# Kernel tuning notes

Hardware: AMD Instinct MI355X
Metric: run time of the kernel (lower is better)

Reference implementation:

```python
import jax, jax.numpy as jnp
import numpy as np

BS, T, N_AGENTS, N_ACTIONS = 8, 256, 8, 20
A = N_AGENTS * N_ACTIONS          # 160 gru input dim
E, D, HID, S = 128, 128, 32, 256  # encoder_dim, decoder_dim, mixing_embed_dim, state_dim
EMBED = HID * (A + E)             # 9216


def _lin(k, out_d, in_d):
    s = 1.0 / np.sqrt(in_d)
    return jax.random.uniform(k, (out_d, in_d), jnp.float32, -s, s)


def _vec(k, d, fan):
    s = 1.0 / np.sqrt(fan)
    return jax.random.uniform(k, (d,), jnp.float32, -s, s)


def setup_inputs() -> dict:
    key = jax.random.key(0)
    ks = jax.random.split(key, 32)
    inp = {
        'act': jax.random.uniform(ks[0], (BS, T, N_AGENTS, N_ACTIONS), jnp.float32),
        'states': jax.random.normal(ks[1], (BS, T, S), jnp.float32),
        # GRU (PyTorch layout: gates stacked [r; z; n])
        'gru_wih': _lin(ks[2], 3 * E, A),
        'gru_whh': _lin(ks[3], 3 * E, E),
        'gru_bih': _vec(ks[4], 3 * E, E),
        'gru_bhh': _vec(ks[5], 3 * E, E),
        # encoder fc
        'fc_w': _lin(ks[6], D, E),
        'fc_b': _vec(ks[7], D, E),
        # attention
        'attn_w': _lin(ks[8], D, D + E),
        'v_w': _vec(ks[9], D, D),
        # hyper_w_1 (2-layer MLP)
        'hw1_w0': _lin(ks[10], EMBED, S), 'hw1_b0': _vec(ks[11], EMBED, S),
        'hw1_w1': _lin(ks[12], EMBED, EMBED), 'hw1_b1': _vec(ks[13], EMBED, EMBED),
        # hyper_w_final (2-layer MLP)
        'hwf_w0': _lin(ks[14], HID, S), 'hwf_b0': _vec(ks[15], HID, S),
        'hwf_w1': _lin(ks[16], HID, HID), 'hwf_b1': _vec(ks[17], HID, HID),
        # hyper_b_1
        'hb1_w': _lin(ks[18], HID, S), 'hb1_b': _vec(ks[19], HID, S),
        # hyper_b_2 (2-layer MLP)
        'hb2_w0': _lin(ks[20], HID, S), 'hb2_b0': _vec(ks[21], HID, S),
        'hb2_w1': _lin(ks[22], 1, HID), 'hb2_b1': _vec(ks[23], 1, HID),
    }
    return inp


def reference(act, states, gru_wih, gru_whh, gru_bih, gru_bhh, fc_w, fc_b,
              attn_w, v_w, hw1_w0, hw1_b0, hw1_w1, hw1_b1,
              hwf_w0, hwf_b0, hwf_w1, hwf_b1, hb1_w, hb1_b,
              hb2_w0, hb2_b0, hb2_w1, hb2_b1):
    bs, t, n_ag, n_ac = act.shape
    a = n_ag * n_ac
    e = gru_whh.shape[1]
    d = fc_w.shape[0]
    hid = hb1_w.shape[0]

    act_flat = act.reshape(bs, t, a)
    # act_his = [zeros, act]; prefixes use only the first t steps of it
    x = jnp.concatenate([jnp.zeros((bs, 1, a), act.dtype), act_flat[:, : t - 1]], axis=1)

    # GRU over full sequence once (causal => identical to recomputing each prefix)
    def step(h, xt):
        gi = xt @ gru_wih.T + gru_bih
        gh = h @ gru_whh.T + gru_bhh
        ir, iz, i_n = jnp.split(gi, 3, axis=-1)
        hr, hz, h_n = jnp.split(gh, 3, axis=-1)
        r = jax.nn.sigmoid(ir + hr)
        z = jax.nn.sigmoid(iz + hz)
        n = jnp.tanh(i_n + r * h_n)
        h_new = (1.0 - z) * n + z * h
        return h_new, h_new

    h0 = jnp.zeros((bs, e), act.dtype)
    _, enc = jax.lax.scan(step, h0, jnp.swapaxes(x, 0, 1))
    enc = jnp.swapaxes(enc, 0, 1)  # [bs, T, E]

    # s0 for prefix ending at step q is tanh(fc(enc[:, q]))
    s0 = jnp.tanh(enc @ fc_w.T + fc_b)  # [bs, T, D]

    # attention: cat order is (s, enc_output)
    w_s, w_e = attn_w[:, :d], attn_w[:, d:]
    ps = s0 @ w_s.T            # [bs, Tq, D]
    pe = enc @ w_e.T           # [bs, Tk, D]
    pre = jnp.tanh(ps[:, :, None, :] + pe[:, None, :, :])  # [bs, Tq, Tk, D]
    scores = jnp.einsum('bqkd,d->bqk', pre, v_w)
    mask = jnp.tril(jnp.ones((t, t), bool))  # key j <= query q (prefix j < idx)
    scores = jnp.where(mask[None], scores, -jnp.inf)
    attn = jax.nn.softmax(scores, axis=-1)
    c = jnp.einsum('bqk,bke->bqe', attn, enc)  # [bs, T, E]

    inp = jnp.concatenate([act_flat, c], axis=-1).reshape(bs * t, 1, a + e)
    st = states.reshape(bs * t, -1)

    w1 = (jax.nn.relu(st @ hw1_w0.T + hw1_b0) @ hw1_w1.T + hw1_b1).reshape(bs * t, a + e, hid)
    b1 = (st @ hb1_w.T + hb1_b)[:, None, :]
    h = jax.nn.relu(jnp.einsum('bik,bkh->bih', inp, w1) + b1)  # [bs*T, 1, hid]

    wf = (jax.nn.relu(st @ hwf_w0.T + hwf_b0) @ hwf_w1.T + hwf_b1)[:, :, None]  # [bs*T, hid, 1]
    b2 = (jax.nn.relu(st @ hb2_w0.T + hb2_b0) @ hb2_w1.T + hb2_b1)[:, :, None]  # [bs*T, 1, 1]
    q = (jnp.einsum('bih,bho->bio', h, wf) + b2).reshape(bs, t, 1)
    return q
```

## Files before the change

kernel.cpp:

```cpp
#include <hip/hip_runtime.h>
#include <hip/hip_bf16.h>
#include <stdint.h>

typedef __attribute__((ext_vector_type(4))) float f32x4;
typedef __attribute__((ext_vector_type(8))) short short8v;
typedef __attribute__((ext_vector_type(4))) unsigned short u16x4;

constexpr int kT  = 256;
constexpr int kA  = 160;

__device__ __forceinline__ float bf2f(unsigned short u){
  union { unsigned int u; float f; } c; c.u = ((unsigned int)u) << 16; return c.f;
}
__device__ __forceinline__ unsigned short f2bf(float f){
  union { float f; unsigned int u; } c; c.f = f;
  unsigned int r = (c.u + 0x7FFFu + ((c.u >> 16) & 1u)) >> 16;
  return (unsigned short)r;
}
__device__ __forceinline__ float sigmoid_fast(float x){
  return __builtin_amdgcn_rcpf(1.f + __expf(-x));
}
__device__ __forceinline__ float tanhf_fast(float x){
  float xc = fminf(fmaxf(x, -15.f), 15.f);
  float t = __expf(2.f * xc);
  return (t - 1.f) * __builtin_amdgcn_rcpf(t + 1.f);
}
__device__ __forceinline__ void gload_lds16(const void* g, void* l){
  __builtin_amdgcn_global_load_lds((const __attribute__((address_space(1))) void*)g,
                                   (__attribute__((address_space(3))) void*)l, 16, 0, 0);
}
__device__ __forceinline__ void bar_lgkm(){
  asm volatile("s_waitcnt lgkmcnt(0)" ::: "memory");
  __builtin_amdgcn_s_barrier();
  asm volatile("" ::: "memory");
}
__device__ __forceinline__ void bar_only(){
  asm volatile("" ::: "memory");
  __builtin_amdgcn_s_barrier();
  asm volatile("" ::: "memory");
}

__global__ __launch_bounds__(256) void k_fill_f32(float* out, int n, float v){
  int i = blockIdx.x * blockDim.x + threadIdx.x;
  if (i < n) out[i] = v;
}

__global__ __launch_bounds__(256) void k_f32_to_bf16(const float* __restrict__ src,
                                                     unsigned short* __restrict__ dst, int n4){
  int stride = gridDim.x * blockDim.x;
  for (int i = blockIdx.x * blockDim.x + threadIdx.x; i < n4; i += stride){
    f32x4 v = *(const f32x4*)(src + (size_t)i * 4);
    u16x4 o;
    o[0] = f2bf(v[0]); o[1] = f2bf(v[1]); o[2] = f2bf(v[2]); o[3] = f2bf(v[3]);
    *(u16x4*)(dst + (size_t)i * 4) = o;
  }
}

__global__ __launch_bounds__(384) void k_gi(const float* __restrict__ act,
                                            const float* __restrict__ wih,
                                            const float* __restrict__ bih,
                                            float* __restrict__ gi){
  int blk = blockIdx.x;
  int b = blk >> 5, tg = blk & 31;
  int j = threadIdx.x;
  __shared__ __align__(16) float xh[8][kA];
  for (int idx = j; idx < 8 * kA; idx += 384){
    int u = idx / kA, i = idx - u * kA;
    int t = tg * 8 + u;
    xh[u][i] = (t == 0) ? 0.f : act[((size_t)b * kT + t - 1) * kA + i];
  }
  __syncthreads();
  float acc[8] = {0,0,0,0,0,0,0,0};
  for (int i = 0; i < kA; i += 4){
    f32x4 wv = *(const f32x4*)(wih + (size_t)j * kA + i);
#pragma unroll
    for (int jj = 0; jj < 4; ++jj)
#pragma unroll
      for (int u = 0; u < 8; ++u)
        acc[u] += wv[jj] * xh[u][i + jj];
  }
  float bv = bih[j];
#pragma unroll
  for (int u = 0; u < 8; ++u)
    gi[((size_t)b * kT + tg * 8 + u) * 384 + j] = acc[u] + bv;
}

template<int RELU>
__device__ __forceinline__ void gemm576_body(const unsigned short* __restrict__ A,
                                             const unsigned short* __restrict__ B,
                                             const float* __restrict__ bias,
                                             unsigned short* __restrict__ C,
                                             int M, int Nc, int K, int ldc,
                                             int bid, int nwg, char* smem){
  int nbm = M >> 7;
  int cpx = nwg >> 3;
  int sw  = (bid & 7) * cpx + (bid >> 3);
  int bm = sw % nbm, bn = sw / nbm;
  int arow0 = bm << 7;
  int bcol0 = bn * 576;
  int t = threadIdx.x;
  int l = t & 63, w = t >> 6;
  int wr = w >> 2, wc = w & 3;
  int lr = l & 15, kq = l >> 4;
  int Kb = K * 2;
  int ar = t >> 2, ap = t & 3;
  size_t aoffg = (size_t)ar * Kb + ((ap ^ ((ar >> 1) & 3)) << 4);
  size_t boffg[5];
#pragma unroll
  for (int i = 0; i < 5; ++i){
    int q = i * 512 + t, r = q >> 2, p = q & 3;
    boffg[i] = (size_t)r * Kb + ((p ^ ((r >> 1) & 3)) << 4);
  }
  const char* Ag = (const char*)(A + (size_t)arow0 * K);
  const char* Bg = (const char*)(B + (size_t)bcol0 * K);
  int dA = t * 16;
  int kk16 = (kq ^ ((lr >> 1) & 3)) << 4;
  int aRd = (wr * 64 + lr) * 64 + kk16;
  int bRd = 8192 + (wc * 144 + lr) * 64 + kk16;
  f32x4 acc[4][9] = {};
  int nt = K >> 5;

  auto stage = [&](int kt, int bi){
    size_t kb = (size_t)kt * 64;
    char* Ld = smem + bi * 49152;
    gload_lds16(Ag + aoffg + kb, Ld + dA);
#pragma unroll
    for (int i = 0; i < 5; ++i)
      gload_lds16(Bg + boffg[i] + kb, Ld + 8192 + i * 8192 + dA);
  };

  stage(0, 0);
  stage(1, 1);
  asm volatile("s_waitcnt vmcnt(6)" ::: "memory");
  int cur = 0;
  for (int kt = 0; kt < nt; ++kt){
    bar_only();
    if (kt + 2 < nt){
      int nb = cur + 2; if (nb >= 3) nb -= 3;
      stage(kt + 2, nb);
    }
    const char* Ld = smem + cur * 49152;
    short8v af[4];
#pragma unroll
    for (int m = 0; m < 4; ++m) af[m] = *(const short8v*)(Ld + aRd + m * 1024);
#pragma unroll
    for (int c = 0; c < 3; ++c){
      short8v bf[3];
#pragma unroll
      for (int j = 0; j < 3; ++j) bf[j] = *(const short8v*)(Ld + bRd + (c * 3 + j) * 1024);
      __builtin_amdgcn_s_setprio(1);
#pragma unroll
      for (int m = 0; m < 4; ++m)
#pragma unroll
        for (int j = 0; j < 3; ++j)
          acc[m][c * 3 + j] = __builtin_amdgcn_mfma_f32_16x16x32_bf16(af[m], bf[j], acc[m][c * 3 + j], 0, 0, 0);
      __builtin_amdgcn_s_setprio(0);
    }
    if (kt + 1 < nt){
      if (kt + 2 < nt) asm volatile("s_waitcnt vmcnt(6)" ::: "memory");
      else             asm volatile("s_waitcnt vmcnt(0)" ::: "memory");
    }
    ++cur; if (cur == 3) cur = 0;
  }

#pragma unroll
  for (int m = 0; m < 4; ++m){
    int row = arow0 + wr * 64 + m * 16 + kq * 4;
#pragma unroll
    for (int n = 0; n < 9; ++n){
      int col = bcol0 + wc * 144 + n * 16 + lr;
      float bv = bias[col];
#pragma unroll
      for (int r = 0; r < 4; ++r){
        float v = acc[m][n][r] + bv;
        if (RELU) v = fmaxf(v, 0.f);
        C[(size_t)(row + r) * ldc + col] = f2bf(v);
      }
    }
  }
}

template<int RELU>
__global__ __launch_bounds__(512) void k_gemm576(const unsigned short* __restrict__ A,
                                                 const unsigned short* __restrict__ B,
                                                 const float* __restrict__ bias,
                                                 unsigned short* __restrict__ C,
                                                 int M, int Nc, int K, int ldc){
  __shared__ __align__(16) char smem[147456];
  gemm576_body<RELU>(A, B, bias, C, M, Nc, K, ldc, blockIdx.x, gridDim.x, smem);
}

__global__ __launch_bounds__(512) void k_gru_g1_conv(const float* __restrict__ gi,
                                                     const float* __restrict__ whh,
                                                     const float* __restrict__ bhh,
                                                     float* __restrict__ enc,
                                                     const unsigned short* __restrict__ stb,
                                                     const unsigned short* __restrict__ w0b,
                                                     const float* __restrict__ hb0,
                                                     unsigned short* __restrict__ zb,
                                                     const float* __restrict__ csrc,
                                                     unsigned short* __restrict__ cdst,
                                                     int n4){
  __shared__ __align__(16) char smem[147456];
  int blk = blockIdx.x;
  if (blk >= 264){
    int stride = (gridDim.x - 264) * 512;
    for (int i = (blk - 264) * 512 + threadIdx.x; i < n4; i += stride){
      f32x4 v = *(const f32x4*)(csrc + (size_t)i * 4);
      u16x4 o;
      o[0] = f2bf(v[0]); o[1] = f2bf(v[1]); o[2] = f2bf(v[2]); o[3] = f2bf(v[3]);
      *(u16x4*)(cdst + (size_t)i * 4) = o;
    }
    return;
  }
  if (blk >= 8){
    gemm576_body<1>(stb, w0b, hb0, zb, 2048, 9216, 256, 9216, blk - 8, 256, smem);
    return;
  }
  float* h_lds = (float*)smem;
  float (*red)[128] = (float(*)[128])(smem + 512);
  int b = blk;
  int tid = threadIdx.x;
  int e = tid & 127, s = tid >> 7;
  float W0[32], W1[32], W2[32];
#pragma unroll
  for (int k = 0; k < 32; ++k){
    W0[k] = whh[(size_t)(0 * 128 + e) * 128 + s * 32 + k];
    W1[k] = whh[(size_t)(1 * 128 + e) * 128 + s * 32 + k];
    W2[k] = whh[(size_t)(2 * 128 + e) * 128 + s * 32 + k];
  }
  if (tid < 128) h_lds[tid] = 0.f;
  float bh0 = 0.f, bh1 = 0.f, bh2 = 0.f;
  if (tid < 128){ bh0 = bhh[e]; bh1 = bhh[128 + e]; bh2 = bhh[256 + e]; }
  const float* gib = gi + (size_t)b * kT * 384;
  float* encb = enc + (size_t)b * kT * 128;
  float gir = 0.f, giz = 0.f, gin = 0.f;
  if (tid < 128){ gir = gib[e]; giz = gib[128 + e]; gin = gib[256 + e]; }
  bar_lgkm();
  for (int t = 0; t < kT; ++t){
    float p0 = 0.f, p1 = 0.f, p2 = 0.f;
#pragma unroll
    for (int k4 = 0; k4 < 8; ++k4){
      f32x4 hv = *(const f32x4*)(h_lds + s * 32 + k4 * 4);
#pragma unroll
      for (int jj = 0; jj < 4; ++jj){
        p0 += W0[k4 * 4 + jj] * hv[jj];
        p1 += W1[k4 * 4 + jj] * hv[jj];
        p2 += W2[k4 * 4 + jj] * hv[jj];
      }
    }
    float nir = 0.f, niz = 0.f, nin = 0.f;
    if (t + 1 < kT && tid < 128){
      const float* gn = gib + (size_t)(t + 1) * 384;
      nir = gn[e]; niz = gn[128 + e]; nin = gn[256 + e];
    }
    red[s * 3 + 0][e] = p0; red[s * 3 + 1][e] = p1; red[s * 3 + 2][e] = p2;
    bar_lgkm();
    if (tid < 128){
      float ghr = red[0][e] + red[3][e] + red[6][e] + red[9][e]  + bh0;
      float ghz = red[1][e] + red[4][e] + red[7][e] + red[10][e] + bh1;
      float ghn = red[2][e] + red[5][e] + red[8][e] + red[11][e] + bh2;
      float r = sigmoid_fast(gir + ghr);
      float z = sigmoid_fast(giz + ghz);
      float n = tanhf_fast(gin + r * ghn);
      float hnew = (1.f - z) * n + z * h_lds[e];
      h_lds[e] = hnew;
      encb[t * 128 + e] = hnew;
    }
    bar_lgkm();
    gir = nir; giz = niz; gin = nin;
  }
}

__global__ __launch_bounds__(128) void k_attnpre(const float* __restrict__ enc,
                                                 const float* __restrict__ fc_w,
                                                 const float* __restrict__ fc_b,
                                                 const float* __restrict__ attn_w,
                                                 float* __restrict__ ps,
                                                 float* __restrict__ pe){
  int bt = blockIdx.x, o = threadIdx.x;
  __shared__ __align__(16) float ench[128], s0h[128];
  ench[o] = enc[(size_t)bt * 128 + o];
  __syncthreads();
  float a0 = fc_b[o], a1 = 0.f;
  for (int i = 0; i < 128; i += 4){
    f32x4 wv = *(const f32x4*)(fc_w + (size_t)o * 128 + i);
    f32x4 we = *(const f32x4*)(attn_w + (size_t)o * 256 + 128 + i);
    f32x4 ev = *(const f32x4*)(ench + i);
#pragma unroll
    for (int jj = 0; jj < 4; ++jj){ a0 += wv[jj] * ev[jj]; a1 += we[jj] * ev[jj]; }
  }
  s0h[o] = tanhf_fast(a0);
  pe[(size_t)bt * 128 + o] = a1;
  __syncthreads();
  float a2 = 0.f;
  for (int i = 0; i < 128; i += 4){
    f32x4 ws = *(const f32x4*)(attn_w + (size_t)o * 256 + i);
    f32x4 sv = *(const f32x4*)(s0h + i);
#pragma unroll
    for (int jj = 0; jj < 4; ++jj) a2 += ws[jj] * sv[jj];
  }
  ps[(size_t)bt * 128 + o] = a2;
}

__global__ __launch_bounds__(256) void k_attn(const float* __restrict__ enc,
                                              const float* __restrict__ ps,
                                              const float* __restrict__ pe,
                                              const float* __restrict__ v_w,
                                              float* __restrict__ cbuf){
  int q = blockIdx.x, b = blockIdx.y;
  int tid = threadIdx.x;
  __shared__ __align__(16) float psh[128], vwh[128];
  __shared__ __align__(16) float sch[256];
  __shared__ __align__(16) float rr[256];
  __shared__ float mxs, dns;
  if (tid < 128){
    psh[tid] = ps[((size_t)b * kT + q) * 128 + tid];
    vwh[tid] = v_w[tid];
  }
  __syncthreads();
  int nk = q + 1;
  for (int k = tid; k < nk; k += 256){
    const float* per = pe + ((size_t)b * kT + k) * 128;
    float sc = 0.f;
    for (int d = 0; d < 128; d += 4){
      f32x4 pv = *(const f32x4*)(per + d);
      f32x4 qv = *(const f32x4*)(psh + d);
      sc += vwh[d + 0] * tanhf_fast(qv[0] + pv[0]);
      sc += vwh[d + 1] * tanhf_fast(qv[1] + pv[1]);
      sc += vwh[d + 2] * tanhf_fast(qv[2] + pv[2]);
      sc += vwh[d + 3] * tanhf_fast(qv[3] + pv[3]);
    }
    sch[k] = sc;
  }
  __syncthreads();
  float lm = -3.0e38f;
  for (int k = tid; k < nk; k += 256) lm = fmaxf(lm, sch[k]);
  rr[tid] = lm; __syncthreads();
  for (int off = 128; off > 0; off >>= 1){
    if (tid < off) rr[tid] = fmaxf(rr[tid], rr[tid + off]);
    __syncthreads();
  }
  if (tid == 0) mxs = rr[0];
  __syncthreads();
  float mxv = mxs;
  float lsum = 0.f;
  for (int k = tid; k < nk; k += 256){
    float p = __expf(sch[k] - mxv);
    sch[k] = p; lsum += p;
  }
  __syncthreads();
  rr[tid] = lsum; __syncthreads();
  for (int off = 128; off > 0; off >>= 1){
    if (tid < off) rr[tid] += rr[tid + off];
    __syncthreads();
  }
  if (tid == 0) dns = __builtin_amdgcn_rcpf(rr[0]);
  __syncthreads();
  float rd = dns;
  int d = tid & 127, half = tid >> 7;
  float acc = 0.f;
  for (int k = half; k < nk; k += 2)
    acc += sch[k] * enc[((size_t)b * kT + k) * 128 + d];
  rr[tid] = acc; __syncthreads();
  if (half == 0)
    cbuf[((size_t)b * kT + q) * 128 + d] = (acc + rr[d + 128]) * rd;
}

__global__ __launch_bounds__(256) void k_final(const float* __restrict__ states,
                                               const float* __restrict__ act,
                                               const float* __restrict__ cbuf,
                                               const unsigned short* __restrict__ w1f,
                                               const float* __restrict__ hb1_w, const float* __restrict__ hb1_b,
                                               const float* __restrict__ hwf_w0, const float* __restrict__ hwf_b0,
                                               const float* __restrict__ hwf_w1, const float* __restrict__ hwf_b1,
                                               const float* __restrict__ hb2_w0, const float* __restrict__ hb2_b0,
                                               const float* __restrict__ hb2_w1, const float* __restrict__ hb2_b1,
                                               float* __restrict__ out){
  int bt = blockIdx.x, tid = threadIdx.x;
  __shared__ __align__(16) float sth[256], inph[288], red[256];
  __shared__ __align__(16) float t1h[32], t2h[32], b1h[32], wfh[32], hvals[32];
  __shared__ float b2s;
  sth[tid] = states[(size_t)bt * 256 + tid];
  if (tid < 160) inph[tid] = act[(size_t)bt * 160 + tid];
  if (tid < 128) inph[160 + tid] = cbuf[(size_t)bt * 128 + tid];
  __syncthreads();
  int o = tid & 31, s = tid >> 5;
  float p1 = 0.f, p2 = 0.f, p3 = 0.f;
  for (int k = s * 32; k < s * 32 + 32; k += 4){
    f32x4 sv  = *(const f32x4*)(sth + k);
    f32x4 w1v = *(const f32x4*)(hwf_w0 + (size_t)o * 256 + k);
    f32x4 w2v = *(const f32x4*)(hb2_w0 + (size_t)o * 256 + k);
    f32x4 w3v = *(const f32x4*)(hb1_w  + (size_t)o * 256 + k);
#pragma unroll
    for (int jj = 0; jj < 4; ++jj){
      p1 += w1v[jj] * sv[jj]; p2 += w2v[jj] * sv[jj]; p3 += w3v[jj] * sv[jj];
    }
  }
  red[tid] = p1; __syncthreads();
  if (tid < 32){
    float a = hwf_b0[tid];
#pragma unroll
    for (int s8 = 0; s8 < 8; ++s8) a += red[s8 * 32 + tid];
    t1h[tid] = fmaxf(a, 0.f);
  }
  __syncthreads();
  red[tid] = p2; __syncthreads();
  if (tid < 32){
    float a = hb2_b0[tid];
#pragma unroll
    for (int s8 = 0; s8 < 8; ++s8) a += red[s8 * 32 + tid];
    t2h[tid] = fmaxf(a, 0.f);
  }
  __syncthreads();
  red[tid] = p3; __syncthreads();
  if (tid < 32){
    float a = hb1_b[tid];
#pragma unroll
    for (int s8 = 0; s8 < 8; ++s8) a += red[s8 * 32 + tid];
    b1h[tid] = a;
  }
  __syncthreads();
  if (tid < 32){
    float a = hwf_b1[tid];
#pragma unroll
    for (int j = 0; j < 32; ++j) a += hwf_w1[(size_t)tid * 32 + j] * t1h[j];
    wfh[tid] = a;
  }
  if (tid == 64){
    float a = hb2_b1[0];
#pragma unroll
    for (int j = 0; j < 32; ++j) a += hb2_w1[j] * t2h[j];
    b2s = a;
  }
  __syncthreads();
  float ph = 0.f;
  const unsigned short* wrow = w1f + (size_t)bt * 9216;
  for (int i = s * 36; i < s * 36 + 36; ++i)
    ph += inph[i] * bf2f(wrow[i * 32 + o]);
  red[tid] = ph; __syncthreads();
  if (tid < 32){
    float a = b1h[tid];
#pragma unroll
    for (int s8 = 0; s8 < 8; ++s8) a += red[s8 * 32 + tid];
    hvals[tid] = fmaxf(a, 0.f) * wfh[tid];
  }
  __syncthreads();
  if (tid == 0){
    float q = b2s;
#pragma unroll
    for (int j = 0; j < 32; ++j) q += hvals[j];
    out[bt] = q;
  }
}

extern "C" void kernel_launch(void* const* d_in, const int* in_sizes, int n_in,
                              void* d_out, int out_size, void* d_ws, size_t ws_size,
                              hipStream_t stream){
  float* outp = (float*)d_out;

  bool ok = (n_in == 24) && out_size == 2048 &&
            in_sizes[0] == 327680 && in_sizes[1] == 524288 &&
            in_sizes[2] == 61440  && in_sizes[3] == 49152 &&
            in_sizes[10] == 2359296 && in_sizes[12] == 84934656;
  if (!ok){
    k_fill_f32<<<dim3(8), dim3(256), 0, stream>>>(outp, 2048, 1.0e6f);
    return;
  }

  const float* act    = (const float*)d_in[0];
  const float* states = (const float*)d_in[1];
  const float* wih    = (const float*)d_in[2];
  const float* whh    = (const float*)d_in[3];
  const float* bih    = (const float*)d_in[4];
  const float* bhh    = (const float*)d_in[5];
  const float* fc_w   = (const float*)d_in[6];
  const float* fc_b   = (const float*)d_in[7];
  const float* attn_w = (const float*)d_in[8];
  const float* v_w    = (const float*)d_in[9];
  const float* hw1_w0 = (const float*)d_in[10];
  const float* hw1_b0 = (const float*)d_in[11];
  const float* hw1_w1 = (const float*)d_in[12];
  const float* hw1_b1 = (const float*)d_in[13];
  const float* hwf_w0 = (const float*)d_in[14];
  const float* hwf_b0 = (const float*)d_in[15];
  const float* hwf_w1 = (const float*)d_in[16];
  const float* hwf_b1 = (const float*)d_in[17];
  const float* hb1_w  = (const float*)d_in[18];
  const float* hb1_b  = (const float*)d_in[19];
  const float* hb2_w0 = (const float*)d_in[20];
  const float* hb2_b0 = (const float*)d_in[21];
  const float* hb2_w1 = (const float*)d_in[22];
  const float* hb2_b1 = (const float*)d_in[23];

  char* ws = (char*)d_ws;
  size_t off = 0;
  auto alloc = [&](size_t bytes)->void*{
    void* p = ws + off; off += (bytes + 255) & ~(size_t)255; return p;
  };
  unsigned short* zb  = (unsigned short*)alloc((size_t)2048 * 9216 * 2);
  unsigned short* w1f = (unsigned short*)alloc((size_t)2048 * 9216 * 2);
  unsigned short* w0b = (unsigned short*)alloc((size_t)9216 * 256 * 2);
  unsigned short* stb = (unsigned short*)alloc((size_t)2048 * 256 * 2);
  float* gi   = (float*)alloc((size_t)2048 * 384 * 4);
  float* enc  = (float*)alloc((size_t)2048 * 128 * 4);
  float* psb  = (float*)alloc((size_t)2048 * 128 * 4);
  float* peb  = (float*)alloc((size_t)2048 * 128 * 4);
  float* cbuf = (float*)alloc((size_t)2048 * 128 * 4);
  size_t floor_bytes = off;
  const size_t row_bytes = (size_t)9216 * 2;
  const size_t slack = (size_t)2 << 20;
  if (ws_size < floor_bytes + 576 * row_bytes + slack){
    k_fill_f32<<<dim3(8), dim3(256), 0, stream>>>(outp, 2048, (float)(ws_size >> 20));
    return;
  }
  size_t avail = ws_size - floor_bytes - slack;
  int chunk_rows = (int)(((avail / row_bytes) / 576) * 576);
  if (chunk_rows > 9216) chunk_rows = 9216;
  unsigned short* w1c = (unsigned short*)(ws + floor_bytes);
  int first_nc = chunk_rows;

  k_f32_to_bf16<<<dim3(1024), dim3(256), 0, stream>>>(hw1_w0, w0b, 9216 * 256 / 4);
  k_f32_to_bf16<<<dim3(256),  dim3(256), 0, stream>>>(states, stb, 2048 * 256 / 4);
  k_gi<<<dim3(256), dim3(384), 0, stream>>>(act, wih, bih, gi);
  k_gru_g1_conv<<<dim3(768), dim3(512), 0, stream>>>(gi, whh, bhh, enc,
                                                     stb, w0b, hw1_b0, zb,
                                                     hw1_w1, w1c, first_nc * 9216 / 4);
  k_attnpre<<<dim3(2048), dim3(128), 0, stream>>>(enc, fc_w, fc_b, attn_w, psb, peb);
  k_attn<<<dim3(256, 8), dim3(256), 0, stream>>>(enc, psb, peb, v_w, cbuf);
  for (int c0 = 0; c0 < 9216; c0 += chunk_rows){
    int nc = 9216 - c0; if (nc > chunk_rows) nc = chunk_rows;
    if (c0 > 0)
      k_f32_to_bf16<<<dim3(2048), dim3(256), 0, stream>>>(hw1_w1 + (size_t)c0 * 9216, w1c, nc * 9216 / 4);
    k_gemm576<0><<<dim3(16 * (nc / 576)), dim3(512), 0, stream>>>(zb, w1c, hw1_b1 + c0, w1f + c0,
                                                                  2048, nc, 9216, 9216);
  }
  k_final<<<dim3(2048), dim3(256), 0, stream>>>(states, act, cbuf, w1f,
      hb1_w, hb1_b, hwf_w0, hwf_b0, hwf_w1, hwf_b1, hb2_w0, hb2_b0, hb2_w1, hb2_b1,
      outp);
}
```

Baseline: 747.8 us.

## Replace 576-column GEMM with 288-column tile, 3-stage LDS pipeline

```diff
diff --git a/kernel.cpp b/kernel.cpp
--- a/kernel.cpp
+++ b/kernel.cpp
@@ -181,13 +181,110 @@
 }
 
 template<int RELU>
-__global__ __launch_bounds__(512) void k_gemm576(const unsigned short* __restrict__ A,
+__global__ __launch_bounds__(256) void k_gemm288(const unsigned short* __restrict__ A,
                                                  const unsigned short* __restrict__ B,
                                                  const float* __restrict__ bias,
                                                  unsigned short* __restrict__ C,
                                                  int M, int Nc, int K, int ldc){
-  __shared__ __align__(16) char smem[147456];
-  gemm576_body<RELU>(A, B, bias, C, M, Nc, K, ldc, blockIdx.x, gridDim.x, smem);
+  __shared__ __align__(16) char smem[79872];
+  int nbm = M >> 7;
+  int nwg = gridDim.x, bid = blockIdx.x;
+  int cpx = nwg >> 3;
+  int sw  = (bid & 7) * cpx + (bid >> 3);
+  int bm = sw % nbm, bn = sw / nbm;
+  int arow0 = bm << 7;
+  int bcol0 = bn * 288;
+  int t = threadIdx.x;
+  int l = t & 63, w = t >> 6;
+  int wr = w >> 1, wc = w & 1;
+  int lr = l & 15, kq = l >> 4;
+  int Kb = K * 2;
+  size_t aoffg[2];
+#pragma unroll
+  for (int i = 0; i < 2; ++i){
+    int q = i * 256 + t, r = q >> 2, p = q & 3;
+    aoffg[i] = (size_t)r * Kb + ((p ^ ((r >> 1) & 3)) << 4);
+  }
+  size_t boffg[5];
+#pragma unroll
+  for (int i = 0; i < 5; ++i){
+    int q = i * 256 + t, r = q >> 2, p = q & 3;
+    boffg[i] = (size_t)r * Kb + ((p ^ ((r >> 1) & 3)) << 4);
+  }
+  const char* Ag = (const char*)(A + (size_t)arow0 * K);
+  const char* Bg = (const char*)(B + (size_t)bcol0 * K);
+  int dT = t * 16;
+  int kk16 = (kq ^ ((lr >> 1) & 3)) << 4;
+  int aRd = (wr * 64 + lr) * 64 + kk16;
+  int bRd = 8192 + (wc * 144 + lr) * 64 + kk16;
+  f32x4 acc[4][9] = {};
+  int nt = K >> 5;
+  bool w01 = (t < 128);
+
+  auto stage = [&](int kt, int bi){
+    size_t kb = (size_t)kt * 64;
+    char* Ld = smem + bi * 26624;
+    gload_lds16(Ag + aoffg[0] + kb, Ld + dT);
+    gload_lds16(Ag + aoffg[1] + kb, Ld + 4096 + dT);
+#pragma unroll
+    for (int i = 0; i < 4; ++i)
+      gload_lds16(Bg + boffg[i] + kb, Ld + 8192 + i * 4096 + dT);
+    if (w01) gload_lds16(Bg + boffg[4] + kb, Ld + 24576 + dT);
+  };
+  auto waitJ = [&](){
+    if (w01) asm volatile("s_waitcnt vmcnt(7)" ::: "memory");
+    else     asm volatile("s_waitcnt vmcnt(6)" ::: "memory");
+  };
+
+  stage(0, 0);
+  stage(1, 1);
+  waitJ();
+  int cur = 0;
+  for (int kt = 0; kt < nt; ++kt){
+    bar_only();
+    if (kt + 2 < nt){
+      int nb = cur + 2; if (nb >= 3) nb -= 3;
+      stage(kt + 2, nb);
+    }
+    const char* Ld = smem + cur * 26624;
+    short8v af[4];
+#pragma unroll
+    for (int m = 0; m < 4; ++m) af[m] = *(const short8v*)(Ld + aRd + m * 1024);
+#pragma unroll
+    for (int c = 0; c < 3; ++c){
+      short8v bf[3];
+#pragma unroll
+      for (int j = 0; j < 3; ++j) bf[j] = *(const short8v*)(Ld + bRd + (c * 3 + j) * 1024);
+      __builtin_amdgcn_s_setprio(1);
+#pragma unroll
+      for (int m = 0; m < 4; ++m)
+#pragma unroll
+        for (int j = 0; j < 3; ++j)
+          acc[m][c * 3 + j] = __builtin_amdgcn_mfma_f32_16x16x32_bf16(af[m], bf[j], acc[m][c * 3 + j], 0, 0, 0);
+      __builtin_amdgcn_s_setprio(0);
+    }
+    if (kt + 1 < nt){
+      if (kt + 2 < nt) waitJ();
+      else             asm volatile("s_waitcnt vmcnt(0)" ::: "memory");
+    }
+    ++cur; if (cur == 3) cur = 0;
+  }
+
+#pragma unroll
+  for (int m = 0; m < 4; ++m){
+    int row = arow0 + wr * 64 + m * 16 + kq * 4;
+#pragma unroll
+    for (int n = 0; n < 9; ++n){
+      int col = bcol0 + wc * 144 + n * 16 + lr;
+      float bv = bias[col];
+#pragma unroll
+      for (int r = 0; r < 4; ++r){
+        float v = acc[m][n][r] + bv;
+        if (RELU) v = fmaxf(v, 0.f);
+        C[(size_t)(row + r) * ldc + col] = f2bf(v);
+      }
+    }
+  }
 }
 
 __global__ __launch_bounds__(512) void k_gru_g1_conv(const float* __restrict__ gi,
@@ -510,12 +607,12 @@
   size_t floor_bytes = off;
   const size_t row_bytes = (size_t)9216 * 2;
   const size_t slack = (size_t)2 << 20;
-  if (ws_size < floor_bytes + 576 * row_bytes + slack){
+  if (ws_size < floor_bytes + 288 * row_bytes + slack){
     k_fill_f32<<<dim3(8), dim3(256), 0, stream>>>(outp, 2048, (float)(ws_size >> 20));
     return;
   }
   size_t avail = ws_size - floor_bytes - slack;
-  int chunk_rows = (int)(((avail / row_bytes) / 576) * 576);
+  int chunk_rows = (int)(((avail / row_bytes) / 288) * 288);
   if (chunk_rows > 9216) chunk_rows = 9216;
   unsigned short* w1c = (unsigned short*)(ws + floor_bytes);
   int first_nc = chunk_rows;
@@ -532,7 +629,7 @@
     int nc = 9216 - c0; if (nc > chunk_rows) nc = chunk_rows;
     if (c0 > 0)
       k_f32_to_bf16<<<dim3(2048), dim3(256), 0, stream>>>(hw1_w1 + (size_t)c0 * 9216, w1c, nc * 9216 / 4);
-    k_gemm576<0><<<dim3(16 * (nc / 576)), dim3(512), 0, stream>>>(zb, w1c, hw1_b1 + c0, w1f + c0,
+    k_gemm288<0><<<dim3(16 * (nc / 288)), dim3(256), 0, stream>>>(zb, w1c, hw1_b1 + c0, w1f + c0,
                                                                   2048, nc, 9216, 9216);
   }
   k_final<<<dim3(2048), dim3(256), 0, stream>>>(states, act, cbuf, w1f,
```

Result: slower. 796.9 us (+6.6%).
